# Kernel optimization log

Hardware: AMD Instinct MI355X
Metric: run time of the kernel (lower is better)

The kernel has to match this reference:

```python
import jax, jax.numpy as jnp
import numpy as np

N = 131072; B = 4; PER = N // B
M = 32768; MPER = M // B; K = 16; E = M * K
NF = 16; C = 32
BNC = float(1.0 / np.sqrt(1.0 + 1e-5))  # BatchNorm1d in eval mode, default running stats (mean=0,var=1,affine=identity)
_kd = np.array([[1.,1.,1.],[-1.,1.,1.],[1.,-1.,1.],[1.,1.,-1.],[-1.,-1.,1.],[-1.,1.,-1.],[1.,-1.,-1.],[-1.,-1.,-1.]], np.float32) / np.float32(np.sqrt(3.0))
KDIRS = jnp.asarray(_kd)  # [8,3] LightKernel directions


def _ln(x, g, b):
    m = x.mean(-1, keepdims=True)
    v = ((x - m) ** 2).mean(-1, keepdims=True)
    return (x - m) / jnp.sqrt(v + 1e-5) * g + b


def _mlp2(x, w1, b1, w2, b2):
    # Seq(Lin, BN, SiLU) x2 ; BN in eval mode == multiply by BNC
    h = jax.nn.silu(BNC * (x @ w1 + b1))
    return jax.nn.silu(BNC * (h @ w2 + b2))


def setup_inputs():
    rng = np.random.default_rng(0)
    f32 = np.float32
    w = lambda fi, fo: jnp.asarray((rng.standard_normal((fi, fo)) * 0.05).astype(f32))
    dg = lambda n: jnp.asarray((rng.standard_normal(n) * 0.05).astype(f32))
    z = lambda n: jnp.zeros((n,), jnp.float32)
    o = lambda n: jnp.ones((n,), jnp.float32)
    pos = jnp.asarray((rng.standard_normal((N, 3)) * 5.0).astype(f32))
    reflectance = jnp.asarray(rng.random(N).astype(f32))
    batch = jnp.asarray(np.repeat(np.arange(B), PER).astype(np.int64))
    sf = jnp.full((B,), 10.0, jnp.float32)
    # voxel-sampled centers: MPER per cloud, within each cloud's index range
    idx = np.concatenate([b * PER + rng.choice(PER, MPER, replace=False) for b in range(B)])
    tb = np.repeat(np.arange(B), MPER)
    # radius-graph edges: K in-batch source neighbors per sampled target
    col = (rng.integers(0, PER, size=(M, K)) + tb[:, None] * PER).reshape(-1)
    row = np.repeat(np.arange(M), K)
    inp = dict(pos=pos, reflectance=reflectance, sf=sf,
               batch=batch, idx=jnp.asarray(idx.astype(np.int64)),
               col=jnp.asarray(col.astype(np.int64)), row=jnp.asarray(row.astype(np.int64)))
    inp.update(stem_ln_g=o(97), stem_ln_b=z(97), stem_w1=w(97, 64), stem_b1=z(64),
               stem_w2=w(64, C), stem_b2=z(C),
               lk_w=w(8, 3), lk_b=z(3), lk_ln_g=o(3), lk_ln_b=z(3),
               loc_w1=w(C + 7, 64), loc_b1=z(64), loc_w2=w(64, 4 * C), loc_b2=z(4 * C),
               exp_w=w(128, 512), exp_b=z(512),
               dw1_w=dg(512), dw1_b=z(512), pw1_w=w(512, 512), pw1_b=z(512),
               dw2_w=dg(512), dw2_b=z(512), pw2_w=w(512, 512), pw2_b=z(512),
               proj_w=w(512, 128), proj_b=z(128))
    return inp


def _forward(pos, reflectance, sf, batch, idx, col, row,
             stem_ln_g, stem_ln_b, stem_w1, stem_b1, stem_w2, stem_b2,
             lk_w, lk_b, lk_ln_g, lk_ln_b,
             loc_w1, loc_b1, loc_w2, loc_b2,
             exp_w, exp_b, dw1_w, dw1_b, pw1_w, pw1_b,
             dw2_w, dw2_b, pw2_w, pw2_b, proj_w, proj_b):
    # --- StemModule: positional encoding + LayerNorm(97) + MLP[97,64,32] ---
    npos = pos / sf[batch][:, None]
    cnt = jax.ops.segment_sum(jnp.ones((N,), jnp.float32), batch, num_segments=B)
    centers = jax.ops.segment_sum(npos, batch, num_segments=B) / jnp.maximum(cnt, 1.0)[:, None]
    npos = npos - centers[batch]
    freqs = 1.0 / (10000.0 ** (2.0 * jnp.arange(NF, dtype=jnp.float32) / NF))
    pe = npos[:, :, None] * freqs                                   # [N,3,NF]
    pe = jnp.concatenate([jnp.sin(pe), jnp.cos(pe)], axis=-1).reshape(N, -1)  # [N,96]
    xin = _ln(jnp.concatenate([pe, reflectance[:, None]], axis=1), stem_ln_g, stem_ln_b)
    x = _mlp2(xin, stem_w1, stem_b1, stem_w2, stem_b2)              # [N,C]
    # --- SAModule: PointNetConv on precomputed radius graph ---
    pos4 = jnp.concatenate([pos, reflectance[:, None]], axis=1)     # [N,4]
    rel = pos4[col] - pos4[idx][row]                                # [E,4] pos_j - pos_i
    rel3 = rel[:, :3]
    dirs = rel3 / (jnp.linalg.norm(rel3, axis=1, keepdims=True) + 1e-8)
    kr = dirs @ KDIRS.T                                             # [E,8] kernel responses
    ecnt = jax.ops.segment_sum(jnp.ones((E,), jnp.float32), row, num_segments=M)
    nb = jax.ops.segment_sum(kr, row, num_segments=M) / jnp.maximum(ecnt, 1.0)[:, None]  # scatter_mean
    sfeat = _ln(nb @ lk_w + lk_b, lk_ln_g, lk_ln_b)                 # [M,3]
    msg = jnp.concatenate([x[col], rel, sfeat[row]], axis=1)        # [E,C+7]
    h = _mlp2(msg, loc_w1, loc_b1, loc_w2, loc_b2)                  # [E,4C] local_nn
    agg = jax.ops.segment_max(h, row, num_segments=M)               # max aggregation [M,4C]
    # --- InvertedResidualBlock (all kernel-size-1 convs => linear / per-channel) ---
    r = agg
    o = jax.nn.silu(BNC * (agg @ exp_w + exp_b))        # expand 128->512
    o = jax.nn.silu(BNC * (o * dw1_w + dw1_b))          # depthwise conv k=1
    o = jax.nn.silu(BNC * (o @ pw1_w + pw1_b))          # pointwise conv
    o = jax.nn.silu(BNC * o)                            # BN+SiLU between DWSep blocks
    o = jax.nn.silu(BNC * (o * dw2_w + dw2_b))
    o = jax.nn.silu(BNC * (o @ pw2_w + pw2_b))
    o = BNC * o                                         # trailing BN (no act)
    o = BNC * (o @ proj_w + proj_b)                     # project 512->128 + BN
    return jax.nn.silu(o + r)                           # [M,4C]


def reference(pos, reflectance, sf, batch, idx, col, row,
              stem_ln_g, stem_ln_b, stem_w1, stem_b1, stem_w2, stem_b2,
              lk_w, lk_b, lk_ln_g, lk_ln_b,
              loc_w1, loc_b1, loc_w2, loc_b2,
              exp_w, exp_b, dw1_w, dw1_b, pw1_w, pw1_b,
              dw2_w, dw2_b, pw2_w, pw2_b, proj_w, proj_b):
    return _forward(pos, reflectance, sf, batch, idx, col, row,
                    stem_ln_g, stem_ln_b, stem_w1, stem_b1, stem_w2, stem_b2,
                    lk_w, lk_b, lk_ln_g, lk_ln_b,
                    loc_w1, loc_b1, loc_w2, loc_b2,
                    exp_w, exp_b, dw1_w, dw1_b, pw1_w, pw1_b,
                    dw2_w, dw2_b, pw2_w, pw2_b, proj_w, proj_b)
```

## Files before the change

### kernel.cpp

```cpp
#include <hip/hip_runtime.h>

typedef unsigned short u16;
typedef unsigned int   u32;
typedef unsigned long long u64;
typedef __attribute__((ext_vector_type(8))) u16  u16x8;
typedef __attribute__((ext_vector_type(4))) float f32x4;

#define N_PTS   131072
#define M_PTS   32768
#define BNCF    0.9999950000374997f

__device__ __forceinline__ float b2f(u16 u) {
    u32 x = ((u32)u) << 16;
    float f;
    __builtin_memcpy(&f, &x, 4);
    return f;
}
__device__ __forceinline__ u16 f2b(float f) {
    u32 x;
    __builtin_memcpy(&x, &f, 4);
    u32 r = x + 0x7fffu + ((x >> 16) & 1u);
    return (u16)(r >> 16);
}
__device__ __forceinline__ u16 f2b_hw(float f) {
    u32 r;
    asm("v_cvt_pk_bf16_f32 %0, %1, %1" : "=v"(r) : "v"(f));
    return (u16)r;
}
__device__ __forceinline__ u32 f2b2(float a, float b) {
    u32 r;
    asm("v_cvt_pk_bf16_f32 %0, %1, %2" : "=v"(r) : "v"(a), "v"(b));
    return r;
}
__device__ __forceinline__ float silu_f(float x) {
    return x * __builtin_amdgcn_rcpf(1.0f + __expf(-x));
}

__device__ __forceinline__ f32x4 mfma_bf16(u16x8 a, u16x8 b, f32x4 c) {
    asm volatile("v_mfma_f32_16x16x32_bf16 %0, %1, %2, %0"
                 : "+v"(c) : "v"(a), "v"(b));
    return c;
}
__device__ __forceinline__ void mai_guard() {
    asm volatile("s_nop 7\n\ts_nop 7\n\ts_nop 3");
}

__device__ __forceinline__ void cp_glds16(const u16* g, u16* l) {
    typedef const __attribute__((address_space(1))) u32* gp1_t;
    typedef __attribute__((address_space(3))) u32* lp3_t;
    __builtin_amdgcn_global_load_lds((gp1_t)(unsigned long long)g,
                                     (lp3_t)(unsigned long long)l, 16, 0, 0);
}

__global__ __launch_bounds__(256) void k_prep(const float* __restrict__ expw, u16* __restrict__ expwt,
                                              const float* __restrict__ pw1w, u16* __restrict__ pw1t,
                                              const float* __restrict__ pw2w, u16* __restrict__ pw2t,
                                              const float* __restrict__ prjw, u16* __restrict__ prjt,
                                              const float* __restrict__ lw1,  u16* __restrict__ lw1t,
                                              const float* __restrict__ lw2,  u16* __restrict__ lw2t,
                                              const float* __restrict__ sw1,  u16* __restrict__ sw1t,
                                              const float* __restrict__ sw2,  u16* __restrict__ sw2t,
                                              float* __restrict__ cent) {
    __shared__ u16 tile[64][66];
    int bid = blockIdx.x;
    if (bid < 160) {
        const float* W; u16* O; int K, Nn, tk, tn_;
        if (bid < 16)              { W = expw; O = expwt; K = 128; Nn = 512; tk = bid >> 3; tn_ = bid & 7; }
        else if ((bid -= 16) < 64) { W = pw1w; O = pw1t;  K = 512; Nn = 512; tk = bid >> 3; tn_ = bid & 7; }
        else if ((bid -= 64) < 64) { W = pw2w; O = pw2t;  K = 512; Nn = 512; tk = bid >> 3; tn_ = bid & 7; }
        else { bid -= 64;            W = prjw; O = prjt;  K = 512; Nn = 128; tk = bid >> 1; tn_ = bid & 1; }
        int k0 = tk * 64, n0 = tn_ * 64;
        int c = threadIdx.x & 63, r0 = threadIdx.x >> 6;
#pragma unroll
        for (int rr = 0; rr < 16; ++rr) {
            int row = r0 * 16 + rr;
            tile[row][c] = f2b(W[(long)(k0 + row) * Nn + n0 + c]);
        }
        __syncthreads();
#pragma unroll
        for (int rr = 0; rr < 16; ++rr) {
            int row = r0 * 16 + rr;
            O[(long)(n0 + row) * K + k0 + c] = tile[c][row];
        }
        return;
    }
    int idx = (bid - 160) * 256 + threadIdx.x;
    if (bid == 247 && threadIdx.x < 16) cent[threadIdx.x] = 0.0f;
    const float* W; u16* O; int K, ksh, Nn;
    if (idx < 4096)                  { W = lw1; O = lw1t; K = 39; ksh = 6; Nn = 64;  }
    else if ((idx -= 4096) < 8192)   { W = lw2; O = lw2t; K = 64; ksh = 6; Nn = 128; }
    else if ((idx -= 8192) < 8192)   { W = sw1; O = sw1t; K = 97; ksh = 7; Nn = 64;  }
    else if ((idx -= 8192) < 2048)   { W = sw2; O = sw2t; K = 64; ksh = 6; Nn = 32;  }
    else return;
    int n = idx >> ksh, k = idx & ((1 << ksh) - 1);
    O[idx] = (k < K) ? f2b(W[(long)k * Nn + n]) : (u16)0;
}

__global__ __launch_bounds__(256) void k_centers(const float* __restrict__ pos,
                                                 const float* __restrict__ sfv,
                                                 const int* __restrict__ batch,
                                                 float* __restrict__ acc) {
    __shared__ float ls[16];
    int t = threadIdx.x, lane = t & 63, wave = t >> 6;
    int i = blockIdx.x * 256 + t;
    int b = batch[blockIdx.x * 256];
    float inv = 1.0f / sfv[b];
    float x = pos[i * 3 + 0] * inv;
    float y = pos[i * 3 + 1] * inv;
    float z = pos[i * 3 + 2] * inv;
#pragma unroll
    for (int m = 1; m < 64; m <<= 1) {
        x += __shfl_xor(x, m);
        y += __shfl_xor(y, m);
        z += __shfl_xor(z, m);
    }
    if (lane == 0) { ls[wave * 4 + 0] = x; ls[wave * 4 + 1] = y; ls[wave * 4 + 2] = z; }
    __syncthreads();
    if (t < 3) {
        float s = ls[t] + ls[4 + t] + ls[8 + t] + ls[12 + t];
        atomicAdd(&acc[b * 4 + t], s);
    }
    if (t == 3) atomicAdd(&acc[b * 4 + 3], 256.0f);
}

__global__ __launch_bounds__(256, 4) void k_stem(const float* __restrict__ pos,
                                              const float* __restrict__ refl,
                                              const float* __restrict__ sfv,
                                              const int* __restrict__ batch,
                                              const float* __restrict__ cacc,
                                              const float* __restrict__ g,
                                              const float* __restrict__ bb,
                                              const u16* __restrict__ w1t,
                                              const float* __restrict__ b1,
                                              const u16* __restrict__ w2t,
                                              const float* __restrict__ b2,
                                              u16* __restrict__ xout) {
    __shared__ u16 xs[128][136];
    const float FLO[8] = {
        1.0f, 0.31622776601683794f, 0.1f, 0.031622776601683791f,
        0.01f, 0.0031622776601683794f, 0.001f, 0.00031622776601683794f};
    const float FHI[8] = {
        0.0001f, 3.1622776601683795e-05f, 1e-05f, 3.1622776601683796e-06f,
        1e-06f, 3.1622776601683797e-07f, 1e-07f, 3.1622776601683792e-08f};
    int t = threadIdx.x;
    int wave = t >> 6, lane = t & 63;
    int quad = lane >> 4, l16 = lane & 15;
    int mt0 = wave * 2;

    {
        int p = t >> 1, half = t & 1;
        int i = blockIdx.x * 128 + p;
        int b = batch[i];
        float s = 1.0f / sfv[b];
        float cnt = fmaxf(cacc[b * 4 + 3], 1.0f);
        float npv[3];
#pragma unroll
        for (int d = 0; d < 3; ++d)
            npv[d] = pos[i * 3 + d] * s - cacc[b * 4 + d] / cnt;

        float fq[8];
#pragma unroll
        for (int f = 0; f < 8; ++f) fq[f] = half ? FHI[f] : FLO[f];

        float sv[3][8], cv[3][8];
        float sum = 0.0f, sq = 0.0f;
#pragma unroll
        for (int d = 0; d < 3; ++d) {
#pragma unroll
            for (int f = 0; f < 8; ++f) {
                float a = npv[d] * fq[f];
                float s_, c_;
                __sincosf(a, &s_, &c_);
                sv[d][f] = s_;
                cv[d][f] = c_;
                sum += s_ + c_;
                sq += s_ * s_ + c_ * c_;
            }
        }
        float rf = refl[i];
        if (half == 0) { sum += rf; sq += rf * rf; }
        sum += __shfl_xor(sum, 1);
        sq  += __shfl_xor(sq, 1);

        float m = sum * (1.0f / 97.0f);
        float var = sq * (1.0f / 97.0f) - m * m;
        float rstd = rsqrtf(fmaxf(var, 0.0f) + 1e-5f);

#pragma unroll
        for (int d = 0; d < 3; ++d) {
            int c0 = d * 32 + half * 8;
            {
                f32x4 g0  = *(const f32x4*)(g + c0);
                f32x4 g1  = *(const f32x4*)(g + c0 + 4);
                f32x4 bb0 = *(const f32x4*)(bb + c0);
                f32x4 bb1 = *(const f32x4*)(bb + c0 + 4);
                u16 tmp[8];
#pragma unroll
                for (int f = 0; f < 4; ++f) {
                    tmp[f]     = f2b_hw((sv[d][f]     - m) * rstd * g0[f] + bb0[f]);
                    tmp[4 + f] = f2b_hw((sv[d][4 + f] - m) * rstd * g1[f] + bb1[f]);
                }
                *(uint4*)(&xs[p][c0]) = *(uint4*)tmp;
            }
            int c1 = d * 32 + 16 + half * 8;
            {
                f32x4 g0  = *(const f32x4*)(g + c1);
                f32x4 g1  = *(const f32x4*)(g + c1 + 4);
                f32x4 bb0 = *(const f32x4*)(bb + c1);
                f32x4 bb1 = *(const f32x4*)(bb + c1 + 4);
                u16 tmp[8];
#pragma unroll
                for (int f = 0; f < 4; ++f) {
                    tmp[f]     = f2b_hw((cv[d][f]     - m) * rstd * g0[f] + bb0[f]);
                    tmp[4 + f] = f2b_hw((cv[d][4 + f] - m) * rstd * g1[f] + bb1[f]);
                }
                *(uint4*)(&xs[p][c1]) = *(uint4*)tmp;
            }
        }
        if (half == 0) {
            float v = rf;
            u16 tmp[8];
            tmp[0] = f2b_hw((v - m) * rstd * g[96] + bb[96]);
#pragma unroll
            for (int f = 1; f < 8; ++f) tmp[f] = 0;
            *(uint4*)(&xs[p][96]) = *(uint4*)tmp;
        } else {
            uint4 z = {0, 0, 0, 0};
            *(uint4*)(&xs[p][104]) = z;
            *(uint4*)(&xs[p][112]) = z;
            *(uint4*)(&xs[p][120]) = z;
        }
    }

    {
        f32x4 acc[2][4];
#pragma unroll
        for (int i = 0; i < 2; ++i)
#pragma unroll
            for (int j = 0; j < 4; ++j) acc[i][j] = (f32x4){0.f, 0.f, 0.f, 0.f};
#pragma unroll
        for (int kk = 0; kk < 128; kk += 32) {
            u16x8 af[2], bfr[4];
#pragma unroll
            for (int i = 0; i < 2; ++i)
                af[i] = *(const u16x8*)(&xs[(mt0 + i) * 16 + l16][kk + quad * 8]);
#pragma unroll
            for (int j = 0; j < 4; ++j)
                bfr[j] = *(const u16x8*)(w1t + (j * 16 + l16) * 128 + kk + quad * 8);
#pragma unroll
            for (int i = 0; i < 2; ++i)
#pragma unroll
                for (int j = 0; j < 4; ++j)
                    acc[i][j] = mfma_bf16(bfr[j], af[i], acc[i][j]);
        }
        mai_guard();
#pragma unroll
        for (int j = 0; j < 4; ++j) {
            f32x4 bv = *(const f32x4*)(b1 + j * 16 + quad * 4);
#pragma unroll
            for (int i = 0; i < 2; ++i) {
                f32x4 c = acc[i][j];
                int mrow = (mt0 + i) * 16 + l16;
                float v0 = silu_f(fmaf(BNCF, c[0], bv[0] * BNCF));
                float v1 = silu_f(fmaf(BNCF, c[1], bv[1] * BNCF));
                float v2 = silu_f(fmaf(BNCF, c[2], bv[2] * BNCF));
                float v3 = silu_f(fmaf(BNCF, c[3], bv[3] * BNCF));
                u32 p2[2] = { f2b2(v0, v1), f2b2(v2, v3) };
                *(u64*)(&xs[mrow][j * 16 + quad * 4]) = *(u64*)p2;
            }
        }
    }

    {
        f32x4 acc[2][2];
#pragma unroll
        for (int i = 0; i < 2; ++i)
#pragma unroll
            for (int j = 0; j < 2; ++j) acc[i][j] = (f32x4){0.f, 0.f, 0.f, 0.f};
#pragma unroll
        for (int kk = 0; kk < 64; kk += 32) {
            u16x8 af[2], bfr[2];
#pragma unroll
            for (int i = 0; i < 2; ++i)
                af[i] = *(const u16x8*)(&xs[(mt0 + i) * 16 + l16][kk + quad * 8]);
#pragma unroll
            for (int j = 0; j < 2; ++j)
                bfr[j] = *(const u16x8*)(w2t + (j * 16 + l16) * 64 + kk + quad * 8);
#pragma unroll
            for (int i = 0; i < 2; ++i)
#pragma unroll
                for (int j = 0; j < 2; ++j)
                    acc[i][j] = mfma_bf16(bfr[j], af[i], acc[i][j]);
        }
        mai_guard();
#pragma unroll
        for (int j = 0; j < 2; ++j) {
            f32x4 bv = *(const f32x4*)(b2 + j * 16 + quad * 4);
#pragma unroll
            for (int i = 0; i < 2; ++i) {
                f32x4 c = acc[i][j];
                int m = (mt0 + i) * 16 + l16;
                long ig = (long)blockIdx.x * 128 + m;
                float v0 = silu_f(fmaf(BNCF, c[0], bv[0] * BNCF));
                float v1 = silu_f(fmaf(BNCF, c[1], bv[1] * BNCF));
                float v2 = silu_f(fmaf(BNCF, c[2], bv[2] * BNCF));
                float v3 = silu_f(fmaf(BNCF, c[3], bv[3] * BNCF));
                u32 p2[2] = { f2b2(v0, v1), f2b2(v2, v3) };
                *(u64*)(xout + ig * 32 + j * 16 + quad * 4) = *(u64*)p2;
            }
        }
    }
}

__global__ __launch_bounds__(256, 4) void k_edge(const float* __restrict__ pos,
                                              const float* __restrict__ refl,
                                              const int* __restrict__ idxp,
                                              const int* __restrict__ colp,
                                              const u16* __restrict__ xfeat,
                                              const float* __restrict__ lkw,
                                              const float* __restrict__ lkb,
                                              const float* __restrict__ lng,
                                              const float* __restrict__ lnb,
                                              const u16* __restrict__ w1t,
                                              const float* __restrict__ b1,
                                              const u16* __restrict__ w2t,
                                              const float* __restrict__ b2,
                                              float* __restrict__ agg,
                                              u16* __restrict__ aggb) {
    __shared__ u16 msgA[128 * 32];
    __shared__ u16 msgB[128 * 32];
    __shared__ u16 ws1[64 * 64];
    __shared__ u16 ws2[128 * 64];
    int t = threadIdx.x;
    int r0 = blockIdx.x * 8;
    long e0 = (long)r0 * 16;
    int wave = t >> 6, lane = t & 63;
    int quad = lane >> 4, l16 = lane & 15;
    int mt0 = wave * 2;

    float b2A[8];
#pragma unroll
    for (int j = 0; j < 8; ++j) b2A[j] = b2[j * 16 + l16] * BNCF;

    if (t >= 128) {
        int gw = (t >> 6) - 2;
#pragma unroll
        for (int it = 0; it < 8; ++it) {
            int cb = it * 128 + gw * 64;
            int ch = cb + lane;
            int row = ch >> 3, sl = ch & 7;
            cp_glds16(w2t + row * 64 + ((sl ^ (row & 7)) << 3), &ws2[cb * 8]);
        }
#pragma unroll
        for (int it = 0; it < 4; ++it) {
            int cb = it * 128 + gw * 64;
            int ch = cb + lane;
            int row = ch >> 3, sl = ch & 7;
            cp_glds16(w1t + row * 64 + ((sl ^ (row & 7)) << 3), &ws1[cb * 8]);
        }
#pragma unroll
        for (int it = 0; it < 4; ++it) {
            int cb = it * 128 + gw * 64;
            int ch = cb + lane;
            int e = ch >> 2, sl = ch & 3;
            int gs = sl ^ (e & 3);
            int c = colp[e0 + e];
            cp_glds16(xfeat + (long)c * 32 + gs * 8, &msgA[cb * 8]);
        }
    } else {
        int e = t;
        int r = r0 + (e >> 4);
        int c = colp[e0 + e];
        int ci = idxp[r];
        float dx = pos[c * 3 + 0] - pos[ci * 3 + 0];
        float dy = pos[c * 3 + 1] - pos[ci * 3 + 1];
        float dz = pos[c * 3 + 2] - pos[ci * 3 + 2];
        float dr = refl[c] - refl[ci];

        float nrm = sqrtf(dx * dx + dy * dy + dz * dz);
        float inv = __builtin_amdgcn_rcpf(nrm + 1e-8f);
        float ux = dx * inv, uy = dy * inv, uz = dz * inv;
#pragma unroll
        for (int msk = 1; msk <= 8; msk <<= 1) {
            ux += __shfl_xor(ux, msk);
            uy += __shfl_xor(uy, msk);
            uz += __shfl_xor(uz, msk);
        }
        const float S3_16 = 0.57735026918962576f * (1.0f / 16.0f);
        const float sxk[8] = {1, -1, 1, 1, -1, -1, 1, -1};
        const float syk[8] = {1, 1, -1, 1, -1, 1, -1, -1};
        const float szk[8] = {1, 1, 1, -1, 1, -1, -1, -1};
        float sc0 = lkb[0], sc1 = lkb[1], sc2 = lkb[2];
#pragma unroll
        for (int j = 0; j < 8; ++j) {
            float nb = (sxk[j] * ux + syk[j] * uy + szk[j] * uz) * S3_16;
            sc0 += nb * lkw[j * 3 + 0];
            sc1 += nb * lkw[j * 3 + 1];
            sc2 += nb * lkw[j * 3 + 2];
        }
        float mm = (sc0 + sc1 + sc2) * (1.0f / 3.0f);
        float vv = ((sc0 - mm) * (sc0 - mm) + (sc1 - mm) * (sc1 - mm) +
                    (sc2 - mm) * (sc2 - mm)) * (1.0f / 3.0f);
        float rstd = rsqrtf(fmaxf(vv, 0.0f) + 1e-5f);

        u16 tmp[8];
        tmp[0] = f2b_hw(dx);
        tmp[1] = f2b_hw(dy);
        tmp[2] = f2b_hw(dz);
        tmp[3] = f2b_hw(dr);
        tmp[4] = f2b_hw((sc0 - mm) * rstd * lng[0] + lnb[0]);
        tmp[5] = f2b_hw((sc1 - mm) * rstd * lng[1] + lnb[1]);
        tmp[6] = f2b_hw((sc2 - mm) * rstd * lng[2] + lnb[2]);
        tmp[7] = 0;
        uint4 z = {0, 0, 0, 0};
        *(uint4*)(&msgB[(e * 4 + (e & 3)) * 8]) = *(uint4*)tmp;
#pragma unroll
        for (int gs = 1; gs < 4; ++gs)
            *(uint4*)(&msgB[(e * 4 + (gs ^ (e & 3))) * 8]) = z;
    }
    __syncthreads();

    {
        f32x4 acc[2][4];
#pragma unroll
        for (int i = 0; i < 2; ++i)
#pragma unroll
            for (int j = 0; j < 4; ++j) acc[i][j] = (f32x4){0.f, 0.f, 0.f, 0.f};
#pragma unroll
        for (int half = 0; half < 2; ++half) {
            u16x8 af[2], bfr[4];
#pragma unroll
            for (int i = 0; i < 2; ++i) {
                int row = (mt0 + i) * 16 + l16;
                const u16* buf = half ? msgB : msgA;
                af[i] = *(const u16x8*)(&buf[(row * 4 + (quad ^ (row & 3))) * 8]);
            }
#pragma unroll
            for (int j = 0; j < 4; ++j) {
                int r = j * 16 + l16;
                int ch = half * 4 + quad;
                bfr[j] = *(const u16x8*)(&ws1[(r * 8 + (ch ^ (r & 7))) * 8]);
            }
#pragma unroll
            for (int i = 0; i < 2; ++i)
#pragma unroll
                for (int j = 0; j < 4; ++j)
                    acc[i][j] = mfma_bf16(bfr[j], af[i], acc[i][j]);
        }
        mai_guard();
#pragma unroll
        for (int j = 0; j < 4; ++j) {
            f32x4 bv = *(const f32x4*)(b1 + j * 16 + quad * 4);
            int n0 = j * 16 + quad * 4;
            int lc = (n0 >> 3) & 3;
            int off = n0 & 7;
            u16* buf = (j < 2) ? msgA : msgB;
#pragma unroll
            for (int i = 0; i < 2; ++i) {
                f32x4 c = acc[i][j];
                int mrow = (mt0 + i) * 16 + l16;
                float v0 = silu_f(fmaf(BNCF, c[0], bv[0] * BNCF));
                float v1 = silu_f(fmaf(BNCF, c[1], bv[1] * BNCF));
                float v2 = silu_f(fmaf(BNCF, c[2], bv[2] * BNCF));
                float v3 = silu_f(fmaf(BNCF, c[3], bv[3] * BNCF));
                u32 p2[2] = { f2b2(v0, v1), f2b2(v2, v3) };
                *(u64*)(&buf[(mrow * 4 + (lc ^ (mrow & 3))) * 8 + off]) = *(u64*)p2;
            }
        }
    }

    {
        f32x4 acc[2][8];
#pragma unroll
        for (int i = 0; i < 2; ++i)
#pragma unroll
            for (int j = 0; j < 8; ++j) acc[i][j] = (f32x4){0.f, 0.f, 0.f, 0.f};
#pragma unroll
        for (int half = 0; half < 2; ++half) {
            u16x8 af[2], bfr[8];
#pragma unroll
            for (int i = 0; i < 2; ++i) {
                int row = (mt0 + i) * 16 + l16;
                const u16* buf = half ? msgB : msgA;
                af[i] = *(const u16x8*)(&buf[(row * 4 + (quad ^ (row & 3))) * 8]);
            }
#pragma unroll
            for (int j = 0; j < 8; ++j) {
                int r = j * 16 + l16;
                int ch = half * 4 + quad;
                bfr[j] = *(const u16x8*)(&ws2[(r * 8 + (ch ^ (r & 7))) * 8]);
            }
#pragma unroll
            for (int i = 0; i < 2; ++i)
#pragma unroll
                for (int j = 0; j < 8; ++j)
                    acc[i][j] = mfma_bf16(af[i], bfr[j], acc[i][j]);
        }
        mai_guard();
#pragma unroll
        for (int i = 0; i < 2; ++i) {
            int rg = r0 + mt0 + i;
#pragma unroll
            for (int j = 0; j < 8; ++j) {
                f32x4 c = acc[i][j];
                int n = j * 16 + l16;
                float mx = fmaxf(fmaxf(c[0], c[1]), fmaxf(c[2], c[3]));
                float mn = fminf(fminf(c[0], c[1]), fminf(c[2], c[3]));
                mx = fmaxf(mx, __shfl_xor(mx, 16));
                mx = fmaxf(mx, __shfl_xor(mx, 32));
                mn = fminf(mn, __shfl_xor(mn, 16));
                mn = fminf(mn, __shfl_xor(mn, 32));
                if (quad == 0) {
                    float v = fmaxf(silu_f(fmaf(BNCF, mx, b2A[j])),
                                    silu_f(fmaf(BNCF, mn, b2A[j])));
                    agg[(long)rg * 128 + n] = v;
                    aggb[(long)rg * 128 + n] = f2b_hw(v);
                }
            }
        }
    }
}

template <int EPI, int OD, int NXB, int K, int Nn>
__global__ __launch_bounds__(256, 4) void k_mgemm(const u16* __restrict__ A,
                                               const u16* __restrict__ Bt,
                                               const float* __restrict__ bias,
                                               const float* __restrict__ dww,
                                               const float* __restrict__ dwb,
                                               const float* __restrict__ res,
                                               void* __restrict__ Ov) {
    __shared__ u16 As[128 * 64];
    __shared__ u16 Bs[128 * 64];
    int t = threadIdx.x;
    int wave = t >> 6, lane = t & 63;
    int quad = lane >> 4, l16 = lane & 15;
    int bx, by;
    if (NXB == 4) {
        int d = blockIdx.x;
        int q = d >> 5, r = d & 31;
        by = q * 8 + (r & 7);
        bx = r >> 3;
    } else {
        bx = 0; by = blockIdx.x;
    }
    int R0 = by * 128, C0 = bx * 128;
    int wm = (wave & 1) * 64, wn = (wave >> 1) * 64;

    int srow = (lane >> 3);
    int sch  = lane & 7;

    f32x4 acc[4][4];
#pragma unroll
    for (int i = 0; i < 4; ++i)
#pragma unroll
        for (int j = 0; j < 4; ++j) acc[i][j] = (f32x4){0.f, 0.f, 0.f, 0.f};

    for (int k0 = 0; k0 < K; k0 += 64) {
#pragma unroll
        for (int it = 0; it < 4; ++it) {
            int base = wave * 32 + it * 8;
            int row = base + srow;
            int gch = (sch ^ (row & 7)) << 3;
            cp_glds16(A  + (long)(R0 + row) * K + k0 + gch, &As[base * 64]);
            cp_glds16(Bt + (long)(C0 + row) * K + k0 + gch, &Bs[base * 64]);
        }
        __syncthreads();
#pragma unroll
        for (int kk = 0; kk < 64; kk += 32) {
            int kb = kk >> 3;
            u16x8 af[4], bfr[4];
#pragma unroll
            for (int tm = 0; tm < 4; ++tm) {
                int r = wm + tm * 16 + l16;
                af[tm] = *(const u16x8*)(&As[r * 64 + (((kb + quad) ^ (r & 7)) << 3)]);
            }
#pragma unroll
            for (int tn = 0; tn < 4; ++tn) {
                int r = wn + tn * 16 + l16;
                bfr[tn] = *(const u16x8*)(&Bs[r * 64 + (((kb + quad) ^ (r & 7)) << 3)]);
            }
#pragma unroll
            for (int tm = 0; tm < 4; ++tm)
#pragma unroll
                for (int tn = 0; tn < 4; ++tn)
                    acc[tm][tn] = mfma_bf16(af[tm], bfr[tn], acc[tm][tn]);
        }
        __syncthreads();
    }

    float bnA[4], dnA[4], dbA[4];
#pragma unroll
    for (int tn = 0; tn < 4; ++tn) {
        int n = C0 + wn + tn * 16 + l16;
        bnA[tn] = bias[n] * BNCF;
        if (EPI == 0 || EPI == 1) { dnA[tn] = dww[n] * BNCF; dbA[tn] = dwb[n] * BNCF; }
        else { dnA[tn] = 0.0f; dbA[tn] = 0.0f; }
    }
    mai_guard();
#pragma unroll
    for (int tm = 0; tm < 4; ++tm) {
#pragma unroll
        for (int tn = 0; tn < 4; ++tn) {
            f32x4 c = acc[tm][tn];
            int n = C0 + wn + tn * 16 + l16;
#pragma unroll
            for (int r = 0; r < 4; ++r) {
                int m = R0 + wm + tm * 16 + quad * 4 + r;
                float v = c[r];
                if (EPI == 0) {
                    v = silu_f(fmaf(BNCF, v, bnA[tn]));
                    v = silu_f(fmaf(v, dnA[tn], dbA[tn]));
                } else if (EPI == 1) {
                    v = silu_f(fmaf(BNCF, v, bnA[tn]));
                    v = silu_f(BNCF * v);
                    v = silu_f(fmaf(v, dnA[tn], dbA[tn]));
                } else if (EPI == 2) {
                    v = silu_f(fmaf(BNCF, v, bnA[tn]));
                    v = BNCF * v;
                } else {
                    v = fmaf(BNCF, v, bnA[tn]);
                    v = silu_f(v + res[(long)m * 128 + n]);
                }
                if (OD == 0)
                    ((u16*)Ov)[(long)m * Nn + n] = f2b_hw(v);
                else
                    ((float*)Ov)[(long)m * Nn + n] = v;
            }
        }
    }
}

extern "C" void kernel_launch(void* const* d_in, const int* in_sizes, int n_in,
                              void* d_out, int out_size, void* d_ws, size_t ws_size,
                              hipStream_t stream) {
    const float* pos   = (const float*)d_in[0];
    const float* refl  = (const float*)d_in[1];
    const float* sfv   = (const float*)d_in[2];
    const int*   batch = (const int*)d_in[3];
    const int*   idxp  = (const int*)d_in[4];
    const int*   colp  = (const int*)d_in[5];
    const float* s_g  = (const float*)d_in[7];
    const float* s_b  = (const float*)d_in[8];
    const float* s_w1 = (const float*)d_in[9];
    const float* s_b1 = (const float*)d_in[10];
    const float* s_w2 = (const float*)d_in[11];
    const float* s_b2 = (const float*)d_in[12];
    const float* lkw  = (const float*)d_in[13];
    const float* lkb  = (const float*)d_in[14];
    const float* lng  = (const float*)d_in[15];
    const float* lnb  = (const float*)d_in[16];
    const float* l_w1 = (const float*)d_in[17];
    const float* l_b1 = (const float*)d_in[18];
    const float* l_w2 = (const float*)d_in[19];
    const float* l_b2 = (const float*)d_in[20];
    const float* expw = (const float*)d_in[21];
    const float* expb = (const float*)d_in[22];
    const float* dw1w = (const float*)d_in[23];
    const float* dw1b = (const float*)d_in[24];
    const float* pw1w = (const float*)d_in[25];
    const float* pw1b = (const float*)d_in[26];
    const float* dw2w = (const float*)d_in[27];
    const float* dw2b = (const float*)d_in[28];
    const float* pw2w = (const float*)d_in[29];
    const float* pw2b = (const float*)d_in[30];
    const float* prjw = (const float*)d_in[31];
    const float* prjb = (const float*)d_in[32];

    char* ws = (char*)d_ws;
    float* cent  = (float*)(ws + 0);
    float* agg   = (float*)(ws + 393280);
    u16*   aggb  = (u16*)(ws + 17170496);
    u16*   u1    = (u16*)(ws + 25559104);
    u16*   u2    = (u16*)(ws + 59113536);
    u16*   xf    = (u16*)(ws + 59113536);
    u16*   expwt = (u16*)(ws + 92667968);
    u16*   pw1t  = (u16*)(ws + 92799040);
    u16*   pw2t  = (u16*)(ws + 93323328);
    u16*   prjt  = (u16*)(ws + 93847616);
    u16*   lw1t  = (u16*)(ws + 93978688);
    u16*   lw2t  = (u16*)(ws + 93986880);
    u16*   sw1t  = (u16*)(ws + 94003264);
    u16*   sw2t  = (u16*)(ws + 94019648);

    k_prep<<<248, 256, 0, stream>>>(expw, expwt, pw1w, pw1t, pw2w, pw2t, prjw, prjt,
                                    l_w1, lw1t, l_w2, lw2t, s_w1, sw1t, s_w2, sw2t,
                                    cent);

    k_centers<<<512, 256, 0, stream>>>(pos, sfv, batch, cent);
    k_stem<<<1024, 256, 0, stream>>>(pos, refl, sfv, batch, cent, s_g, s_b,
                                     sw1t, s_b1, sw2t, s_b2, xf);
    k_edge<<<4096, 256, 0, stream>>>(pos, refl, idxp, colp, xf,
                                     lkw, lkb, lng, lnb,
                                     lw1t, l_b1, lw2t, l_b2, agg, aggb);

    dim3 blk(256);
    k_mgemm<0, 0, 4, 128, 512><<<1024, blk, 0, stream>>>(aggb, expwt, expb, dw1w, dw1b,
                                                         nullptr, u1);
    k_mgemm<1, 0, 4, 512, 512><<<1024, blk, 0, stream>>>(u1, pw1t, pw1b, dw2w, dw2b,
                                                         nullptr, u2);
    k_mgemm<2, 0, 4, 512, 512><<<1024, blk, 0, stream>>>(u2, pw2t, pw2b, nullptr, nullptr,
                                                         nullptr, u1);
    k_mgemm<3, 1, 1, 512, 128><<<256, blk, 0, stream>>>(u1, prjt, prjb, nullptr, nullptr,
                                                        agg, d_out);
}
```

Measured before the change: 286.2 us.

## Double-buffer GEMM LDS tiles with 32-wide K steps to overlap loads

```diff
diff --git a/kernel.cpp b/kernel.cpp
--- a/kernel.cpp
+++ b/kernel.cpp
@@ -529,8 +529,8 @@
                                                const float* __restrict__ dwb,
                                                const float* __restrict__ res,
                                                void* __restrict__ Ov) {
-    __shared__ u16 As[128 * 64];
-    __shared__ u16 Bs[128 * 64];
+    __shared__ u16 As[2][128 * 32];
+    __shared__ u16 Bs[2][128 * 32];
     int t = threadIdx.x;
     int wave = t >> 6, lane = t & 63;
     int quad = lane >> 4, l16 = lane & 15;
@@ -546,8 +546,8 @@
     int R0 = by * 128, C0 = bx * 128;
     int wm = (wave & 1) * 64, wn = (wave >> 1) * 64;
 
-    int srow = (lane >> 3);
-    int sch  = lane & 7;
+    int srow = lane >> 2;
+    int sch  = lane & 3;
 
     f32x4 acc[4][4];
 #pragma unroll
@@ -555,37 +555,49 @@
 #pragma unroll
         for (int j = 0; j < 4; ++j) acc[i][j] = (f32x4){0.f, 0.f, 0.f, 0.f};
 
-    for (int k0 = 0; k0 < K; k0 += 64) {
-#pragma unroll
-        for (int it = 0; it < 4; ++it) {
-            int base = wave * 32 + it * 8;
-            int row = base + srow;
-            int gch = (sch ^ (row & 7)) << 3;
-            cp_glds16(A  + (long)(R0 + row) * K + k0 + gch, &As[base * 64]);
-            cp_glds16(Bt + (long)(C0 + row) * K + k0 + gch, &Bs[base * 64]);
-        }
+#pragma unroll
+    for (int it = 0; it < 2; ++it) {
+        int rb = wave * 32 + it * 16;
+        int row = rb + srow;
+        int gs = (sch ^ ((row ^ (row >> 2)) & 3)) << 3;
+        cp_glds16(A  + (long)(R0 + row) * K + gs, &As[0][rb * 32]);
+        cp_glds16(Bt + (long)(C0 + row) * K + gs, &Bs[0][rb * 32]);
+    }
+
+    constexpr int NSTEP = K / 32;
+#pragma unroll
+    for (int s = 0; s < NSTEP; ++s) {
+        const int cur = s & 1;
         __syncthreads();
-#pragma unroll
-        for (int kk = 0; kk < 64; kk += 32) {
-            int kb = kk >> 3;
-            u16x8 af[4], bfr[4];
-#pragma unroll
-            for (int tm = 0; tm < 4; ++tm) {
-                int r = wm + tm * 16 + l16;
-                af[tm] = *(const u16x8*)(&As[r * 64 + (((kb + quad) ^ (r & 7)) << 3)]);
-            }
-#pragma unroll
-            for (int tn = 0; tn < 4; ++tn) {
-                int r = wn + tn * 16 + l16;
-                bfr[tn] = *(const u16x8*)(&Bs[r * 64 + (((kb + quad) ^ (r & 7)) << 3)]);
-            }
-#pragma unroll
-            for (int tm = 0; tm < 4; ++tm)
-#pragma unroll
-                for (int tn = 0; tn < 4; ++tn)
-                    acc[tm][tn] = mfma_bf16(af[tm], bfr[tn], acc[tm][tn]);
-        }
-        __syncthreads();
+        if (s + 1 < NSTEP) {
+            int k0n = (s + 1) * 32;
+#pragma unroll
+            for (int it = 0; it < 2; ++it) {
+                int rb = wave * 32 + it * 16;
+                int row = rb + srow;
+                int gs = (sch ^ ((row ^ (row >> 2)) & 3)) << 3;
+                cp_glds16(A  + (long)(R0 + row) * K + k0n + gs, &As[cur ^ 1][rb * 32]);
+                cp_glds16(Bt + (long)(C0 + row) * K + k0n + gs, &Bs[cur ^ 1][rb * 32]);
+            }
+        }
+        u16x8 af[4], bfr[4];
+#pragma unroll
+        for (int tm = 0; tm < 4; ++tm) {
+            int r = wm + tm * 16 + l16;
+            int slot = quad ^ ((r ^ (r >> 2)) & 3);
+            af[tm] = *(const u16x8*)(&As[cur][(r * 4 + slot) * 8]);
+        }
+#pragma unroll
+        for (int tn = 0; tn < 4; ++tn) {
+            int r = wn + tn * 16 + l16;
+            int slot = quad ^ ((r ^ (r >> 2)) & 3);
+            bfr[tn] = *(const u16x8*)(&Bs[cur][(r * 4 + slot) * 8]);
+        }
+#pragma unroll
+        for (int tm = 0; tm < 4; ++tm)
+#pragma unroll
+            for (int tn = 0; tn < 4; ++tn)
+                acc[tm][tn] = mfma_bf16(af[tm], bfr[tn], acc[tm][tn]);
     }
 
     float bnA[4], dnA[4], dbA[4];
```

Result: faster. 279.5 us (-2.3%).
